# Optimization experiments

Hardware: AMD Instinct MI355X
Metric: run time of the kernel (lower is better)

## Reference

```python
import jax, jax.numpy as jnp
import numpy as np

NB, HD, NL, NF = 5, 64, 4, 10           # num_bins, hidden_dim(d_model), num_layers, num_frames
DI, DS, DC, DTR = 128, 16, 4, 4          # d_inner=2*HD, d_state, d_conv, dt_rank=ceil(HD/16)
B, H, W = 4, 64, 64


def _conv2d(x, w, b):
    y = jax.lax.conv_general_dilated(x, w, (1, 1), 'SAME',
                                     dimension_numbers=('NCHW', 'OIHW', 'NCHW'))
    return y + b[None, :, None, None]


def _bn_relu(x, gamma, beta, eps=1e-5):
    # BatchNorm2d in training mode: biased batch stats over (N,H,W)
    mean = x.mean(axis=(0, 2, 3), keepdims=True)
    var = x.var(axis=(0, 2, 3), keepdims=True)
    y = (x - mean) * jax.lax.rsqrt(var + eps)
    return jax.nn.relu(y * gamma[None, :, None, None] + beta[None, :, None, None])


def _silu(x):
    return x * jax.nn.sigmoid(x)


def _causal_dwconv(x, w, b):
    # x: (B,L,DI), w: (DI,K) depthwise causal conv, b: (DI,)
    K = w.shape[1]
    L = x.shape[1]
    xp = jnp.pad(x, ((0, 0), (K - 1, 0), (0, 0)))
    y = sum(xp[:, k:k + L, :] * w[:, k] for k in range(K))
    return y + b


def _selective_scan(u, delta, A, Bm, Cm, D):
    # u,delta: (B,L,DI); A: (DI,DS); Bm,Cm: (B,L,DS); D: (DI,)
    dT, BT, CT, uT = (t.transpose(1, 0, 2) for t in (delta, Bm, Cm, u))
    h0 = jnp.zeros((u.shape[0], A.shape[0], A.shape[1]), u.dtype)

    def step(h, inp):
        d_t, B_t, C_t, u_t = inp                     # (B,DI),(B,DS),(B,DS),(B,DI)
        dA = jnp.exp(d_t[:, :, None] * A)            # (B,DI,DS)
        h = dA * h + (d_t * u_t)[:, :, None] * B_t[:, None, :]
        y = jnp.einsum('bds,bs->bd', h, C_t)
        return h, y

    _, ys = jax.lax.scan(step, h0, (dT, BT, CT, uT))  # ys: (L,B,DI)
    return ys.transpose(1, 0, 2) + u * D


def _mamba(x, in_proj, conv_w, conv_b, x_proj, dt_w, dt_b, A_log, Dp, out_proj):
    xz = x @ in_proj.T                               # (B,L,2*DI)
    xi, z = jnp.split(xz, 2, axis=-1)
    xi = _silu(_causal_dwconv(xi, conv_w, conv_b))
    xdbc = xi @ x_proj.T                             # (B,L,DTR+2*DS)
    dt, Bm, Cm = jnp.split(xdbc, [DTR, DTR + DS], axis=-1)
    delta = jax.nn.softplus(dt @ dt_w.T + dt_b)
    A = -jnp.exp(A_log)
    y = _selective_scan(xi, delta, A, Bm, Cm, Dp)
    return (y * _silu(z)) @ out_proj.T


def setup_inputs() -> dict:
    key = jax.random.key(0)
    ks = jax.random.split(key, 20)
    s = 0.02
    inp = {
        'x': jax.random.normal(ks[0], (B, NB, H, W), jnp.float32),
        'enc_w': jax.random.normal(ks[1], (HD, NB, 3, 3), jnp.float32) * s,
        'enc_b': jnp.zeros((HD,), jnp.float32),
        'enc_g': jnp.ones((HD,), jnp.float32),
        'enc_be': jnp.zeros((HD,), jnp.float32),
        'in_proj': jax.random.normal(ks[2], (NL, 2 * DI, HD), jnp.float32) * s,
        'conv_w': jax.random.normal(ks[3], (NL, DI, DC), jnp.float32) * s,
        'conv_b': jnp.zeros((NL, DI), jnp.float32),
        'x_proj': jax.random.normal(ks[4], (NL, DTR + 2 * DS, DI), jnp.float32) * s,
        'dt_w': jax.random.normal(ks[5], (NL, DI, DTR), jnp.float32) * s,
        'dt_b': jax.random.normal(ks[6], (NL, DI), jnp.float32) * 0.1 - 4.0,
        'A_log': jnp.broadcast_to(jnp.log(jnp.arange(1, DS + 1, dtype=jnp.float32)),
                                  (NL, DI, DS)).copy(),
        'Dp': jnp.ones((NL, DI), jnp.float32),
        'out_proj': jax.random.normal(ks[7], (NL, HD, DI), jnp.float32) * s,
        'dec1_w': jax.random.normal(ks[8], (HD, HD, 3, 3), jnp.float32) * s,
        'dec1_b': jnp.zeros((HD,), jnp.float32),
        'dec1_g': jnp.ones((HD,), jnp.float32),
        'dec1_be': jnp.zeros((HD,), jnp.float32),
        'dec2_w': jax.random.normal(ks[9], (NF, HD, 3, 3), jnp.float32) * s,
        'dec2_b': jnp.zeros((NF,), jnp.float32),
    }
    return inp


def reference(x, enc_w, enc_b, enc_g, enc_be, in_proj, conv_w, conv_b, x_proj,
              dt_w, dt_b, A_log, Dp, out_proj, dec1_w, dec1_b, dec1_g, dec1_be,
              dec2_w, dec2_b):
    Bb, _, Hh, Ww = x.shape
    h = _bn_relu(_conv2d(x, enc_w, enc_b), enc_g, enc_be)   # (B,HD,H,W)
    t = h.reshape(Bb, HD, Hh * Ww).transpose(0, 2, 1)        # (B,L,HD)
    for i in range(NL):
        t = t + _mamba(t, in_proj[i], conv_w[i], conv_b[i], x_proj[i],
                       dt_w[i], dt_b[i], A_log[i], Dp[i], out_proj[i])
    h = t.transpose(0, 2, 1).reshape(Bb, HD, Hh, Ww)
    h = _bn_relu(_conv2d(h, dec1_w, dec1_b), dec1_g, dec1_be)
    return _conv2d(h, dec2_w, dec2_b)                        # (B,NF,H,W)
```

## Files before the change

kernel.cpp:

```cpp
#include <hip/hip_runtime.h>
#include <hip/hip_bf16.h>

#define BB   4
#define NBC  5
#define HD   64
#define NLAYER 4
#define NFC  10
#define DIM  128
#define DSN  16
#define DCN  4
#define DTRK 4
#define HH   64
#define WWD  64
#define LL   4096
#define MM   (BB*LL)
#define NCHUNK 128
#define CLEN   32
#define TSTEP  16

__global__ void k_prep_all(const float* __restrict__ in_proj, const float* __restrict__ out_proj,
                           const float* __restrict__ dec1_w, const float* __restrict__ dec2_w,
                           float* __restrict__ wTin, float* __restrict__ wTout,
                           float* __restrict__ wT1, float* __restrict__ wT2,
                           float* __restrict__ stats, float* __restrict__ stats2) {
    int idx = blockIdx.x * blockDim.x + threadIdx.x;
    if (idx < 65536) {
        int n = idx & 255, k = (idx >> 8) & 63, l = idx >> 14;
        wTin[idx] = in_proj[(l << 14) + (n << 6) + k];
    } else if (idx < 98304) {
        int j = idx - 65536;
        int n = j & 63, k = (j >> 6) & 127, l = j >> 13;
        wTout[j] = out_proj[(l << 13) + (n << 7) + k];
    } else if (idx < 135168) {
        int j = idx - 98304;
        int co = j & 63, tap = (j >> 6) % 9, ci = j / 576;
        wT1[j] = dec1_w[co * 576 + ci * 9 + tap];
    } else if (idx < 142848) {
        int j = idx - 135168;
        int tap = j % 12, t2 = j / 12, co = t2 % NFC, ci = t2 / NFC;
        wT2[j] = (tap < 9) ? dec2_w[co * 576 + ci * 9 + tap] : 0.f;
    } else if (idx < 143104) {
        int j = idx - 142848;
        if (j < 128) stats[j] = 0.f; else stats2[j - 128] = 0.f;
    }
}

__global__ void k_enc_conv(const float* __restrict__ x, const float* __restrict__ w,
                           const float* __restrict__ bias, float* __restrict__ out,
                           float* __restrict__ stats) {
    __shared__ float r1[256], r2[256];
    int tid = threadIdx.x;
    int idx = blockIdx.x * 256 + tid;
    int wx = idx & 63;
    int hy = (idx >> 6) & 63;
    int co = (idx >> 12) & 63;
    int b  = idx >> 18;
    float acc = bias[co];
    for (int ci = 0; ci < NBC; ++ci) {
        const float* xin = x + (((long)(b * NBC + ci)) << 12);
        const float* wp  = w + (co * NBC + ci) * 9;
        #pragma unroll
        for (int kh = 0; kh < 3; ++kh) {
            int ih = hy + kh - 1;
            if (ih < 0 || ih >= HH) continue;
            #pragma unroll
            for (int kw = 0; kw < 3; ++kw) {
                int iw = wx + kw - 1;
                if (iw < 0 || iw >= WWD) continue;
                acc += xin[(ih << 6) + iw] * wp[kh * 3 + kw];
            }
        }
    }
    out[idx] = acc;
    r1[tid] = acc; r2[tid] = acc * acc;
    __syncthreads();
    for (int off = 128; off > 0; off >>= 1) {
        if (tid < off) { r1[tid] += r1[tid + off]; r2[tid] += r2[tid + off]; }
        __syncthreads();
    }
    if (tid == 0) {
        atomicAdd(&stats[co], r1[0]);
        atomicAdd(&stats[64 + co], r2[0]);
    }
}

__global__ __launch_bounds__(256, 1) void k_gemm_in_bn(const float* __restrict__ src,
                                                       const float* __restrict__ stats,
                                                       const float* __restrict__ g,
                                                       const float* __restrict__ be,
                                                       const float* __restrict__ wT,
                                                       float* __restrict__ tout,
                                                       float* __restrict__ xz) {
    __shared__ __align__(16) float ts[64 * 68];
    __shared__ float sc[64], sh[64];
    long m0 = (long)blockIdx.x << 6;
    int b = (int)(m0 >> 12);
    int hw0 = (int)(m0 & 4095);
    int tid = threadIdx.x;
    if (tid < 64) {
        float m = stats[tid] * (1.f / 16384.f);
        float var = stats[64 + tid] * (1.f / 16384.f) - m * m;
        float ss = g[tid] * rsqrtf(var + 1e-5f);
        sc[tid] = ss; sh[tid] = be[tid] - m * ss;
    }
    __syncthreads();
    for (int i = tid; i < 4096; i += 256) {
        int pix = i & 63, c = i >> 6;
        float v = src[(((long)((b << 6) + c)) << 12) + hw0 + pix];
        ts[pix * 68 + c] = fmaxf(v * sc[c] + sh[c], 0.f);
    }
    __syncthreads();
    for (int i = tid; i < 4096; i += 256) {
        int r = i >> 6, c = i & 63;
        tout[(m0 + r) * 64 + c] = ts[r * 68 + c];
    }
    int rg = tid >> 5;
    int cg = tid & 31;
    float acc[8][8] = {};
    int n0 = cg << 3;
    for (int k4 = 0; k4 < 16; ++k4) {
        float4 a[8];
        #pragma unroll
        for (int r2 = 0; r2 < 8; ++r2)
            a[r2] = *(const float4*)&ts[((rg << 3) + r2) * 68 + (k4 << 2)];
        #pragma unroll
        for (int kk = 0; kk < 4; ++kk) {
            const float* wr = wT + (((k4 << 2) + kk) << 8) + n0;
            float4 w0 = *(const float4*)&wr[0];
            float4 w1 = *(const float4*)&wr[4];
            #pragma unroll
            for (int r2 = 0; r2 < 8; ++r2) {
                float av = (kk == 0) ? a[r2].x : (kk == 1) ? a[r2].y
                         : (kk == 2) ? a[r2].z : a[r2].w;
                acc[r2][0] += av * w0.x; acc[r2][1] += av * w0.y;
                acc[r2][2] += av * w0.z; acc[r2][3] += av * w0.w;
                acc[r2][4] += av * w1.x; acc[r2][5] += av * w1.y;
                acc[r2][6] += av * w1.z; acc[r2][7] += av * w1.w;
            }
        }
    }
    #pragma unroll
    for (int r2 = 0; r2 < 8; ++r2) {
        long m = m0 + (rg << 3) + r2;
        *(float4*)&xz[(m << 8) + n0]     = make_float4(acc[r2][0], acc[r2][1], acc[r2][2], acc[r2][3]);
        *(float4*)&xz[(m << 8) + n0 + 4] = make_float4(acc[r2][4], acc[r2][5], acc[r2][6], acc[r2][7]);
    }
}

__global__ __launch_bounds__(256, 2) void k_xproj_fused(
        const float* __restrict__ xz, const float* __restrict__ cw,
        const float* __restrict__ cb, const float* __restrict__ Wx,
        const float* __restrict__ dw, const float* __restrict__ dbias,
        const float* __restrict__ A_log,
        float* __restrict__ xi, float* __restrict__ xdbc,
        float* __restrict__ delta, float* __restrict__ Pb, float* __restrict__ Sb) {
    __shared__ float xz_s[35 * 132];
    __shared__ float xi_s[32 * 132];
    __shared__ float w_s[36 * 132];
    __shared__ float xs[32 * 40];
    __shared__ float cwT[4 * 128];
    __shared__ float cb_s[128];
    long m0 = (long)blockIdx.x << 5;
    int l0 = (int)(m0 & 4095);
    int b = (int)(m0 >> 12);
    int chunk = l0 >> 5;
    int tid = threadIdx.x;

    for (int i = tid; i < 35 * 128; i += 256) {
        int j = i >> 7, k = i & 127;
        int l = l0 - 3 + j;
        float v = 0.f;
        if (l >= 0) v = xz[(m0 - 3 + j) * 256 + k];
        xz_s[j * 132 + k] = v;
    }
    if (tid < 128) cb_s[tid] = cb[tid];
    for (int i = tid; i < 512; i += 256) {
        int kk = i >> 7, di = i & 127;
        cwT[(kk << 7) + di] = cw[(di << 2) + kk];
    }
    for (int i = tid; i < 4608; i += 256) {
        int n = i >> 7, k = i & 127;
        w_s[n * 132 + k] = Wx[i];
    }
    __syncthreads();

    for (int ii = 0; ii < 4; ++ii) {
        int i = tid + (ii << 8);
        int r = i >> 5;
        int d4 = (i & 31) << 2;
        float4 a = *(const float4*)&cb_s[d4];
        #pragma unroll
        for (int kk = 0; kk < 4; ++kk) {
            float4 xv = *(const float4*)&xz_s[(r + kk) * 132 + d4];
            float4 wv = *(const float4*)&cwT[(kk << 7) + d4];
            a.x += xv.x * wv.x; a.y += xv.y * wv.y;
            a.z += xv.z * wv.z; a.w += xv.w * wv.w;
        }
        a.x = a.x / (1.f + __expf(-a.x));
        a.y = a.y / (1.f + __expf(-a.y));
        a.z = a.z / (1.f + __expf(-a.z));
        a.w = a.w / (1.f + __expf(-a.w));
        *(float4*)&xi_s[r * 132 + d4] = a;
        *(float4*)&xi[(m0 + r) * 128 + d4] = a;
    }
    __syncthreads();

    int n = tid & 63;
    int rg = tid >> 6;
    if (n < 36) {
        float acc[8] = {0,0,0,0,0,0,0,0};
        for (int k4 = 0; k4 < 32; ++k4) {
            float4 w4 = *(const float4*)&w_s[n * 132 + (k4 << 2)];
            #pragma unroll
            for (int r = 0; r < 8; ++r) {
                float4 a4 = *(const float4*)&xi_s[((rg << 3) + r) * 132 + (k4 << 2)];
                acc[r] += a4.x * w4.x + a4.y * w4.y + a4.z * w4.z + a4.w * w4.w;
            }
        }
        #pragma unroll
        for (int r = 0; r < 8; ++r) {
            int rr = (rg << 3) + r;
            xdbc[(m0 + rr) * 36 + n] = acc[r];
            xs[rr * 40 + n] = acc[r];
        }
    }
    __syncthreads();

    float* delta_s = xz_s;
    for (int i = tid; i < 4096; i += 256) {
        int r = i >> 7, di = i & 127;
        float v = dbias[di];
        float4 d4 = *(const float4*)&dw[di << 2];
        v += xs[r * 40 + 0] * d4.x + xs[r * 40 + 1] * d4.y
           + xs[r * 40 + 2] * d4.z + xs[r * 40 + 3] * d4.w;
        float sp = (v > 20.f) ? v : log1pf(expf(v));
        delta[(m0 + r) * 128 + di] = sp;
        delta_s[r * 132 + di] = sp;
    }
    __syncthreads();

    {
        int di = tid >> 1;
        int dso = (tid & 1) << 3;
        float4 al0 = *(const float4*)&A_log[(di << 4) + dso];
        float4 al1 = *(const float4*)&A_log[(di << 4) + dso + 4];
        float Av[8] = { -expf(al0.x), -expf(al0.y), -expf(al0.z), -expf(al0.w),
                        -expf(al1.x), -expf(al1.y), -expf(al1.z), -expf(al1.w) };
        float h[8] = {0,0,0,0,0,0,0,0};
        float P[8] = {1,1,1,1,1,1,1,1};
        #pragma unroll 4
        for (int i = 0; i < CLEN; ++i) {
            float d = delta_s[i * 132 + di];
            float u = xi_s[i * 132 + di];
            float du = d * u;
            float4 B0 = *(float4*)&xs[i * 40 + DTRK + dso];
            float4 B1 = *(float4*)&xs[i * 40 + DTRK + dso + 4];
            float a0 = __expf(d * Av[0]); h[0] = a0 * h[0] + du * B0.x; P[0] *= a0;
            float a1 = __expf(d * Av[1]); h[1] = a1 * h[1] + du * B0.y; P[1] *= a1;
            float a2 = __expf(d * Av[2]); h[2] = a2 * h[2] + du * B0.z; P[2] *= a2;
            float a3 = __expf(d * Av[3]); h[3] = a3 * h[3] + du * B0.w; P[3] *= a3;
            float a4 = __expf(d * Av[4]); h[4] = a4 * h[4] + du * B1.x; P[4] *= a4;
            float a5 = __expf(d * Av[5]); h[5] = a5 * h[5] + du * B1.y; P[5] *= a5;
            float a6 = __expf(d * Av[6]); h[6] = a6 * h[6] + du * B1.z; P[6] *= a6;
            float a7 = __expf(d * Av[7]); h[7] = a7 * h[7] + du * B1.w; P[7] *= a7;
        }
        long o = (((long)chunk * BB + b) << 11) + (di << 4) + dso;
        *(float4*)&Pb[o]     = make_float4(P[0], P[1], P[2], P[3]);
        *(float4*)&Pb[o + 4] = make_float4(P[4], P[5], P[6], P[7]);
        *(float4*)&Sb[o]     = make_float4(h[0], h[1], h[2], h[3]);
        *(float4*)&Sb[o + 4] = make_float4(h[4], h[5], h[6], h[7]);
    }
}

__global__ void k_scan_p2(float* Pb, const float* __restrict__ Sb) {
    int t = blockIdx.x * blockDim.x + threadIdx.x;
    int b = t >> 11;
    int s = t & 2047;
    float h = 0.f;
    for (int c = 0; c < NCHUNK; ++c) {
        long idx = (((long)c * BB + b) << 11) + s;
        float p = Pb[idx];
        float sv = Sb[idx];
        Pb[idx] = h;
        h = p * h + sv;
    }
}

__global__ __launch_bounds__(256, 1) void k_scan_p3_oi(
        const float* __restrict__ delta, const float* __restrict__ xi,
        const float* __restrict__ xdbc, const float* __restrict__ A_log,
        const float* __restrict__ Dp, const float* __restrict__ xz,
        const float* __restrict__ hin, const float* __restrict__ wTo,
        const float* __restrict__ wTi, float* __restrict__ tio,
        float* __restrict__ xz_out, int doB) {
    __shared__ __align__(16) float d_s[32 * 132];
    __shared__ __align__(16) float u_s[32 * 132];
    __shared__ __align__(16) float bc_s[32 * 36];
    __shared__ __align__(16) float t_s[32 * 68];
    int chunk = blockIdx.x, b = blockIdx.y;
    int tid = threadIdx.x;
    long t0 = ((long)b << 12) + (long)chunk * CLEN;

    for (int i = tid; i < 1024; i += 256) {
        int r = i >> 5, c4 = (i & 31) << 2;
        *(float4*)&d_s[r * 132 + c4] = *(const float4*)&delta[(t0 + r) * 128 + c4];
        *(float4*)&u_s[r * 132 + c4] = *(const float4*)&xi[(t0 + r) * 128 + c4];
    }
    {
        int r = tid >> 3, c4 = (tid & 7) << 2;
        *(float4*)&bc_s[r * 36 + c4] = *(const float4*)&xdbc[(t0 + r) * 36 + DTRK + c4];
    }

    int di = tid >> 1;
    int dso = (tid & 1) << 3;
    float4 al0 = *(const float4*)&A_log[(di << 4) + dso];
    float4 al1 = *(const float4*)&A_log[(di << 4) + dso + 4];
    float Av[8] = { -expf(al0.x), -expf(al0.y), -expf(al0.z), -expf(al0.w),
                    -expf(al1.x), -expf(al1.y), -expf(al1.z), -expf(al1.w) };
    float Dv = Dp[di];
    long o = (((long)chunk * BB + b) << 11) + (di << 4) + dso;
    float4 h0 = *(const float4*)&hin[o];
    float4 h1 = *(const float4*)&hin[o + 4];
    float h[8] = { h0.x, h0.y, h0.z, h0.w, h1.x, h1.y, h1.z, h1.w };
    __syncthreads();

    #pragma unroll 4
    for (int i = 0; i < CLEN; ++i) {
        float d = d_s[i * 132 + di];
        float u = u_s[i * 132 + di];
        float du = d * u;
        const float* bc = &bc_s[i * 36];
        float4 B0 = *(const float4*)&bc[dso];
        float4 B1 = *(const float4*)&bc[dso + 4];
        float4 C0 = *(const float4*)&bc[16 + dso];
        float4 C1 = *(const float4*)&bc[16 + dso + 4];
        float a0 = __expf(d * Av[0]); h[0] = a0 * h[0] + du * B0.x;
        float a1 = __expf(d * Av[1]); h[1] = a1 * h[1] + du * B0.y;
        float a2 = __expf(d * Av[2]); h[2] = a2 * h[2] + du * B0.z;
        float a3 = __expf(d * Av[3]); h[3] = a3 * h[3] + du * B0.w;
        float a4 = __expf(d * Av[4]); h[4] = a4 * h[4] + du * B1.x;
        float a5 = __expf(d * Av[5]); h[5] = a5 * h[5] + du * B1.y;
        float a6 = __expf(d * Av[6]); h[6] = a6 * h[6] + du * B1.z;
        float a7 = __expf(d * Av[7]); h[7] = a7 * h[7] + du * B1.w;
        float yp = h[0] * C0.x + h[1] * C0.y + h[2] * C0.z + h[3] * C0.w
                 + h[4] * C1.x + h[5] * C1.y + h[6] * C1.z + h[7] * C1.w;
        yp += __shfl_xor(yp, 1);
        if (dso == 0)
            u_s[i * 132 + di] = yp + u * Dv;
    }
    __syncthreads();

    for (int i = tid; i < 1024; i += 256) {
        int r = i >> 5, c4 = (i & 31) << 2;
        float4 y4 = *(float4*)&u_s[r * 132 + c4];
        float4 z4 = *(const float4*)&xz[((t0 + r) << 8) + DIM + c4];
        y4.x *= z4.x / (1.f + __expf(-z4.x));
        y4.y *= z4.y / (1.f + __expf(-z4.y));
        y4.z *= z4.z / (1.f + __expf(-z4.z));
        y4.w *= z4.w / (1.f + __expf(-z4.w));
        *(float4*)&u_s[r * 132 + c4] = y4;
    }
    __syncthreads();

    {
        int rg = tid >> 4, cg = tid & 15;
        int n0 = cg << 2;
        float acc[2][4] = {};
        for (int k4 = 0; k4 < 32; ++k4) {
            float4 a0 = *(const float4*)&u_s[(rg << 1) * 132 + (k4 << 2)];
            float4 a1 = *(const float4*)&u_s[((rg << 1) + 1) * 132 + (k4 << 2)];
            #pragma unroll
            for (int kk = 0; kk < 4; ++kk) {
                const float* wr = wTo + (((k4 << 2) + kk) << 6) + n0;
                float4 w0 = *(const float4*)&wr[0];
                float av0 = (kk == 0) ? a0.x : (kk == 1) ? a0.y : (kk == 2) ? a0.z : a0.w;
                float av1 = (kk == 0) ? a1.x : (kk == 1) ? a1.y : (kk == 2) ? a1.z : a1.w;
                acc[0][0] += av0 * w0.x; acc[0][1] += av0 * w0.y;
                acc[0][2] += av0 * w0.z; acc[0][3] += av0 * w0.w;
                acc[1][0] += av1 * w0.x; acc[1][1] += av1 * w0.y;
                acc[1][2] += av1 * w0.z; acc[1][3] += av1 * w0.w;
            }
        }
        #pragma unroll
        for (int r2 = 0; r2 < 2; ++r2) {
            long m = t0 + (rg << 1) + r2;
            float4 tv = *(const float4*)&tio[(m << 6) + n0];
            tv.x += acc[r2][0]; tv.y += acc[r2][1];
            tv.z += acc[r2][2]; tv.w += acc[r2][3];
            *(float4*)&tio[(m << 6) + n0] = tv;
            *(float4*)&t_s[((rg << 1) + r2) * 68 + n0] = tv;
        }
    }
    if (!doB) return;
    __syncthreads();

    {
        int rg = tid >> 5, cgn = tid & 31;
        int n0 = cgn << 3;
        float acc[4][8] = {};
        for (int k4 = 0; k4 < 16; ++k4) {
            float4 a[4];
            #pragma unroll
            for (int r2 = 0; r2 < 4; ++r2)
                a[r2] = *(const float4*)&t_s[((rg << 2) + r2) * 68 + (k4 << 2)];
            #pragma unroll
            for (int kk = 0; kk < 4; ++kk) {
                const float* wr = wTi + (((k4 << 2) + kk) << 8) + n0;
                float4 w0 = *(const float4*)&wr[0];
                float4 w1 = *(const float4*)&wr[4];
                #pragma unroll
                for (int r2 = 0; r2 < 4; ++r2) {
                    float av = (kk == 0) ? a[r2].x : (kk == 1) ? a[r2].y
                             : (kk == 2) ? a[r2].z : a[r2].w;
                    acc[r2][0] += av * w0.x; acc[r2][1] += av * w0.y;
                    acc[r2][2] += av * w0.z; acc[r2][3] += av * w0.w;
                    acc[r2][4] += av * w1.x; acc[r2][5] += av * w1.y;
                    acc[r2][6] += av * w1.z; acc[r2][7] += av * w1.w;
                }
            }
        }
        #pragma unroll
        for (int r2 = 0; r2 < 4; ++r2) {
            long m = t0 + (rg << 2) + r2;
            *(float4*)&xz_out[(m << 8) + n0]     = make_float4(acc[r2][0], acc[r2][1], acc[r2][2], acc[r2][3]);
            *(float4*)&xz_out[(m << 8) + n0 + 4] = make_float4(acc[r2][4], acc[r2][5], acc[r2][6], acc[r2][7]);
        }
    }
}

__global__ __launch_bounds__(256, 1) void k_dec1_new(const float* __restrict__ tin,
                                                     const float* __restrict__ wT,
                                                     const float* __restrict__ bias,
                                                     float* __restrict__ out,
                                                     float* __restrict__ stats2) {
    __shared__ __align__(16) float x_s[64 * 132];
    __shared__ __align__(16) float w_s[4 * 4608];
    int tile = blockIdx.x;
    int b = blockIdx.y;
    int ty0 = (tile >> 3) << 3;
    int tx0 = (tile & 7) << 3;
    int tid = threadIdx.x;
    int wv = tid >> 6;
    int lane = tid & 63;
    int r = lane >> 3;
    int cg = lane & 7;

    for (int i = tid; i < 6400; i += 256) {
        int pl = i >> 6;
        int c = i & 63;
        int py = pl / 10, px = pl - py * 10;
        int ih = ty0 + py - 1, iw = tx0 + px - 1;
        float v = 0.f;
        if (ih >= 0 && ih < HH && iw >= 0 && iw < WWD)
            v = tin[(((long)((b << 12) + (ih << 6) + iw)) << 6) + c];
        x_s[c * 132 + py * 12 + px] = v;
    }
    float* myw = &w_s[wv * 4608];
    const float* gw = wT + (wv * 16) * 576;
    float4 pref[18];
    #pragma unroll
    for (int i = 0; i < 18; ++i)
        pref[i] = *(const float4*)&gw[(i * 64 + lane) * 4];
    #pragma unroll
    for (int i = 0; i < 18; ++i)
        *(float4*)&myw[(i * 64 + lane) * 4] = pref[i];
    __syncthreads();

    float acc[8][8] = {};
    #pragma unroll
    for (int ch = 0; ch < 2; ++ch) {
        if (ch == 0) {
            const float* gw1 = wT + (wv * 16 + 8) * 576;
            #pragma unroll
            for (int i = 0; i < 18; ++i)
                pref[i] = *(const float4*)&gw1[(i * 64 + lane) * 4];
        }
        for (int cl = 0; cl < 8; ++cl) {
            int cib = wv * 16 + ch * 8 + cl;
            float xrow[3][10];
            #pragma unroll
            for (int kh = 0; kh < 3; ++kh) {
                const float* xr = &x_s[cib * 132 + (r + kh) * 12];
                float4 a0 = *(const float4*)&xr[0];
                float4 a1 = *(const float4*)&xr[4];
                float2 a2 = *(const float2*)&xr[8];
                xrow[kh][0] = a0.x; xrow[kh][1] = a0.y; xrow[kh][2] = a0.z; xrow[kh][3] = a0.w;
                xrow[kh][4] = a1.x; xrow[kh][5] = a1.y; xrow[kh][6] = a1.z; xrow[kh][7] = a1.w;
                xrow[kh][8] = a2.x; xrow[kh][9] = a2.y;
            }
            const float* wp = &myw[cl * 576];
            #pragma unroll
            for (int kh = 0; kh < 3; ++kh) {
                #pragma unroll
                for (int kw = 0; kw < 3; ++kw) {
                    const float* wp2 = wp + (kh * 3 + kw) * 64 + (cg << 3);
                    float4 wa = *(const float4*)&wp2[0];
                    float4 wb = *(const float4*)&wp2[4];
                    #pragma unroll
                    for (int j = 0; j < 8; ++j) {
                        float xv = xrow[kh][kw + j];
                        acc[j][0] += xv * wa.x; acc[j][1] += xv * wa.y;
                        acc[j][2] += xv * wa.z; acc[j][3] += xv * wa.w;
                        acc[j][4] += xv * wb.x; acc[j][5] += xv * wb.y;
                        acc[j][6] += xv * wb.z; acc[j][7] += xv * wb.w;
                    }
                }
            }
        }
        if (ch == 0) {
            #pragma unroll
            for (int i = 0; i < 18; ++i)
                *(float4*)&myw[(i * 64 + lane) * 4] = pref[i];
        }
    }

    #pragma unroll
    for (int j = 0; j < 8; ++j) {
        *(float4*)&myw[lane * 68 + (j << 3)]     = make_float4(acc[j][0], acc[j][1], acc[j][2], acc[j][3]);
        *(float4*)&myw[lane * 68 + (j << 3) + 4] = make_float4(acc[j][4], acc[j][5], acc[j][6], acc[j][7]);
    }
    __syncthreads();

    float bv = bias[lane];
    float ssum = 0.f, ssq = 0.f;
    #pragma unroll
    for (int pp = 0; pp < 16; ++pp) {
        int pr = (wv << 1) + (pp >> 3);
        int pc = pp & 7;
        int ol = (pr << 3) + (lane >> 3);
        int ix = (pc << 3) + (lane & 7);
        float s = w_s[ol * 68 + ix] + w_s[4608 + ol * 68 + ix]
                + w_s[9216 + ol * 68 + ix] + w_s[13824 + ol * 68 + ix] + bv;
        out[(((long)((b << 12) + ((ty0 + pr) << 6) + tx0 + pc)) << 6) + lane] = s;
        ssum += s; ssq += s * s;
    }
    float* red = x_s;
    red[(wv << 6) + lane] = ssum;
    red[256 + (wv << 6) + lane] = ssq;
    __syncthreads();
    if (tid < 64) {
        float a = red[tid] + red[64 + tid] + red[128 + tid] + red[192 + tid];
        float q = red[256 + tid] + red[320 + tid] + red[384 + tid] + red[448 + tid];
        atomicAdd(&stats2[tid], a);
        atomicAdd(&stats2[64 + tid], q);
    }
}

__global__ void k_dec2_fused(const float* __restrict__ src, const float* __restrict__ stats2,
                             const float* __restrict__ g, const float* __restrict__ be,
                             const float* __restrict__ wT, const float* __restrict__ bias,
                             float* __restrict__ out) {
    __shared__ float x_s[64 * 101];
    __shared__ float w_s[64 * NFC * 12];
    __shared__ float sc_s[64];
    __shared__ float sh_s[64];
    int tile = blockIdx.x;
    int b = blockIdx.y;
    int ty0 = (tile >> 3) << 3;
    int tx0 = (tile & 7) << 3;
    int tid = threadIdx.x;

    if (tid < 64) {
        float m = stats2[tid] * (1.f / 16384.f);
        float var = stats2[64 + tid] * (1.f / 16384.f) - m * m;
        float s = g[tid] * rsqrtf(var + 1e-5f);
        sc_s[tid] = s;
        sh_s[tid] = be[tid] - m * s;
    }
    for (int i = tid; i < 64 * NFC * 12; i += 256)
        w_s[i] = wT[i];
    __syncthreads();

    for (int i = tid; i < 6400; i += 256) {
        int pl = i >> 6;
        int c = i & 63;
        int py = pl / 10, px = pl - py * 10;
        int ih = ty0 + py - 1, iw = tx0 + px - 1;
        float v = 0.f;
        if (ih >= 0 && ih < HH && iw >= 0 && iw < WWD) {
            v = src[((long)((b << 12) + (ih << 6) + iw)) * 64 + c];
            v = fmaxf(v * sc_s[c] + sh_s[c], 0.f);
        }
        x_s[c * 101 + pl] = v;
    }
    __syncthreads();

    int px = tid & 63;
    int py = px >> 3, pxx = px & 7;
    int cog = tid >> 6;
    float acc[3] = {0.f, 0.f, 0.f};
    int nco = (cog < 2) ? 3 : 2;

    for (int ci = 0; ci < 64; ++ci) {
        const float* xr = &x_s[ci * 101 + py * 10 + pxx];
        float xv[9];
        #pragma unroll
        for (int kh = 0; kh < 3; ++kh)
            #pragma unroll
            for (int kw = 0; kw < 3; ++kw)
                xv[kh * 3 + kw] = xr[kh * 10 + kw];
        #pragma unroll
        for (int j = 0; j < 3; ++j) {
            if (j >= nco) break;
            int co = cog + (j << 2);
            const float* wp = &w_s[(ci * NFC + co) * 12];
            float4 w0 = *(const float4*)&wp[0];
            float4 w1 = *(const float4*)&wp[4];
            float  w8 = wp[8];
            acc[j] += xv[0] * w0.x + xv[1] * w0.y + xv[2] * w0.z + xv[3] * w0.w
                    + xv[4] * w1.x + xv[5] * w1.y + xv[6] * w1.z + xv[7] * w1.w
                    + xv[8] * w8;
        }
    }
    int hw = ((ty0 + py) << 6) + tx0 + pxx;
    #pragma unroll
    for (int j = 0; j < 3; ++j) {
        if (j >= nco) break;
        int co = cog + (j << 2);
        out[((long)(b * NFC + co) << 12) + hw] = acc[j] + bias[co];
    }
}

extern "C" void kernel_launch(void* const* d_in, const int* in_sizes, int n_in,
                              void* d_out, int out_size, void* d_ws, size_t ws_size,
                              hipStream_t stream) {
    const float* x       = (const float*)d_in[0];
    const float* enc_w   = (const float*)d_in[1];
    const float* enc_b   = (const float*)d_in[2];
    const float* enc_g   = (const float*)d_in[3];
    const float* enc_be  = (const float*)d_in[4];
    const float* in_proj = (const float*)d_in[5];
    const float* conv_w  = (const float*)d_in[6];
    const float* conv_b  = (const float*)d_in[7];
    const float* x_proj  = (const float*)d_in[8];
    const float* dt_w    = (const float*)d_in[9];
    const float* dt_b    = (const float*)d_in[10];
    const float* A_log   = (const float*)d_in[11];
    const float* Dp      = (const float*)d_in[12];
    const float* out_prj = (const float*)d_in[13];
    const float* dec1_w  = (const float*)d_in[14];
    const float* dec1_b  = (const float*)d_in[15];
    const float* dec1_g  = (const float*)d_in[16];
    const float* dec1_be = (const float*)d_in[17];
    const float* dec2_w  = (const float*)d_in[18];
    const float* dec2_b  = (const float*)d_in[19];
    float* out = (float*)d_out;

    float* ws = (float*)d_ws;
    size_t off = 0;
    float* conv_buf  = ws + off; off += 1048576;
    float* stats     = ws + off; off += 128;
    float* stats2    = ws + off; off += 128;
    float* wT1       = ws + off; off += 36864;
    float* wT2       = ws + off; off += 7680;
    float* wTin      = ws + off; off += 65536;
    float* wTout     = ws + off; off += 32768;
    float* t_buf     = ws + off; off += 1048576;
    float* xz_buf    = ws + off; off += 4194304;
    float* xi_buf    = ws + off; off += 2097152;
    float* xdbc_buf  = ws + off; off += 589824;
    float* delta_buf = ws + off; off += 2097152;
    float* Sb_buf    = ws + off; off += 1048576;
    (void)ws_size; (void)in_sizes; (void)n_in; (void)out_size;

    float* Pb = conv_buf;
    float* Sb = Sb_buf;

    k_prep_all<<<560, 256, 0, stream>>>(in_proj, out_prj, dec1_w, dec2_w,
                                        wTin, wTout, wT1, wT2, stats, stats2);

    k_enc_conv<<<4096, 256, 0, stream>>>(x, enc_w, enc_b, conv_buf, stats);

    k_gemm_in_bn<<<256, 256, 0, stream>>>(conv_buf, stats, enc_g, enc_be, wTin, t_buf, xz_buf);
    dim3 pg(NCHUNK, BB);
    for (int i = 0; i < NLAYER; ++i) {
        k_xproj_fused<<<512, 256, 0, stream>>>(xz_buf, conv_w + i * DIM * DCN,
                                               conv_b + i * DIM, x_proj + i * 36 * DIM,
                                               dt_w + i * DIM * DTRK, dt_b + i * DIM,
                                               A_log + i * DIM * DSN,
                                               xi_buf, xdbc_buf, delta_buf, Pb, Sb);
        k_scan_p2<<<32, 256, 0, stream>>>(Pb, Sb);
        int doB = (i < NLAYER - 1) ? 1 : 0;
        k_scan_p3_oi<<<pg, 256, 0, stream>>>(delta_buf, xi_buf, xdbc_buf,
                                             A_log + i * DIM * DSN, Dp + i * DIM,
                                             xz_buf, Pb, wTout + i * 8192,
                                             wTin + ((i + 1) & 3) * 16384,
                                             t_buf, xz_buf, doB);
    }

    dim3 dg1(64, BB);
    k_dec1_new<<<dg1, 256, 0, stream>>>(t_buf, wT1, dec1_b, conv_buf, stats2);
    k_dec2_fused<<<dg1, 256, 0, stream>>>(conv_buf, stats2, dec1_g, dec1_be, wT2, dec2_b, out);
}
```

Baseline: 490.9 us.

## Recompute conv/delta in scan pass and shrink chunks with halo buffers

Stops writing xi and delta to global memory and recomputes the causal depthwise conv, SiLU and softplus delta inside the scan output kernel. Because xz is overwritten in place by the next layer's in-projection, the last three rows of each 16-step subchunk are saved to ping-pong halo buffers for the conv window. Chunk length drops from 32 to 16, giving twice as many blocks, with occupancy hints raised. The aim is to cut global memory traffic and improve parallelism, at the cost of duplicated arithmetic and a sequential inter-chunk pass that is now twice as long.

```diff
diff --git a/kernel.cpp b/kernel.cpp
--- a/kernel.cpp
+++ b/kernel.cpp
@@ -14,9 +14,9 @@
 #define WWD  64
 #define LL   4096
 #define MM   (BB*LL)
-#define NCHUNK 128
-#define CLEN   32
-#define TSTEP  16
+#define SUB    16
+#define NSUB   256
+#define WIN    19
 
 __global__ void k_prep_all(const float* __restrict__ in_proj, const float* __restrict__ out_proj,
                            const float* __restrict__ dec1_w, const float* __restrict__ dec2_w,
@@ -90,7 +90,8 @@
                                                        const float* __restrict__ be,
                                                        const float* __restrict__ wT,
                                                        float* __restrict__ tout,
-                                                       float* __restrict__ xz) {
+                                                       float* __restrict__ xz,
+                                                       float* __restrict__ halo0) {
     __shared__ __align__(16) float ts[64 * 68];
     __shared__ float sc[64], sh[64];
     long m0 = (long)blockIdx.x << 6;
@@ -142,100 +143,106 @@
     #pragma unroll
     for (int r2 = 0; r2 < 8; ++r2) {
         long m = m0 + (rg << 3) + r2;
-        *(float4*)&xz[(m << 8) + n0]     = make_float4(acc[r2][0], acc[r2][1], acc[r2][2], acc[r2][3]);
-        *(float4*)&xz[(m << 8) + n0 + 4] = make_float4(acc[r2][4], acc[r2][5], acc[r2][6], acc[r2][7]);
-    }
-}
-
-__global__ __launch_bounds__(256, 2) void k_xproj_fused(
+        float4 v0 = make_float4(acc[r2][0], acc[r2][1], acc[r2][2], acc[r2][3]);
+        float4 v1 = make_float4(acc[r2][4], acc[r2][5], acc[r2][6], acc[r2][7]);
+        *(float4*)&xz[(m << 8) + n0]     = v0;
+        *(float4*)&xz[(m << 8) + n0 + 4] = v1;
+        int lr = (int)(m & 15);
+        if (lr >= 13 && n0 < 128) {
+            int bb = (int)(m >> 12), scc = ((int)m & 4095) >> 4;
+            long ho = (((long)bb * NSUB + scc) * 3 + (lr - 13)) * 128 + n0;
+            *(float4*)&halo0[ho]     = v0;
+            *(float4*)&halo0[ho + 4] = v1;
+        }
+    }
+}
+
+__global__ __launch_bounds__(256, 3) void k_xproj_fused(
         const float* __restrict__ xz, const float* __restrict__ cw,
         const float* __restrict__ cb, const float* __restrict__ Wx,
         const float* __restrict__ dw, const float* __restrict__ dbias,
         const float* __restrict__ A_log,
-        float* __restrict__ xi, float* __restrict__ xdbc,
-        float* __restrict__ delta, float* __restrict__ Pb, float* __restrict__ Sb) {
-    __shared__ float xz_s[35 * 132];
-    __shared__ float xi_s[32 * 132];
-    __shared__ float w_s[36 * 132];
-    __shared__ float xs[32 * 40];
-    __shared__ float cwT[4 * 128];
-    __shared__ float cb_s[128];
-    long m0 = (long)blockIdx.x << 5;
+        float* __restrict__ xdbc, float* __restrict__ Pb, float* __restrict__ Sb) {
+    __shared__ __align__(16) float xz_s[WIN * 128];
+    __shared__ __align__(16) float xi_s[SUB * 128];
+    __shared__ __align__(16) float w_s[36 * 132];
+    __shared__ __align__(16) float xs[SUB * 36];
+    long m0 = (long)blockIdx.x << 4;
     int l0 = (int)(m0 & 4095);
     int b = (int)(m0 >> 12);
-    int chunk = l0 >> 5;
+    int sc = l0 >> 4;
     int tid = threadIdx.x;
 
-    for (int i = tid; i < 35 * 128; i += 256) {
-        int j = i >> 7, k = i & 127;
+    for (int i = tid; i < WIN * 32; i += 256) {
+        int j = i >> 5, c4 = (i & 31) << 2;
+        float4 v = make_float4(0.f, 0.f, 0.f, 0.f);
         int l = l0 - 3 + j;
-        float v = 0.f;
-        if (l >= 0) v = xz[(m0 - 3 + j) * 256 + k];
-        xz_s[j * 132 + k] = v;
-    }
-    if (tid < 128) cb_s[tid] = cb[tid];
-    for (int i = tid; i < 512; i += 256) {
-        int kk = i >> 7, di = i & 127;
-        cwT[(kk << 7) + di] = cw[(di << 2) + kk];
-    }
-    for (int i = tid; i < 4608; i += 256) {
-        int n = i >> 7, k = i & 127;
-        w_s[n * 132 + k] = Wx[i];
-    }
-    __syncthreads();
-
-    for (int ii = 0; ii < 4; ++ii) {
-        int i = tid + (ii << 8);
-        int r = i >> 5;
-        int d4 = (i & 31) << 2;
-        float4 a = *(const float4*)&cb_s[d4];
-        #pragma unroll
-        for (int kk = 0; kk < 4; ++kk) {
-            float4 xv = *(const float4*)&xz_s[(r + kk) * 132 + d4];
-            float4 wv = *(const float4*)&cwT[(kk << 7) + d4];
-            a.x += xv.x * wv.x; a.y += xv.y * wv.y;
-            a.z += xv.z * wv.z; a.w += xv.w * wv.w;
-        }
+        if (l >= 0) v = *(const float4*)&xz[(m0 - 3 + j) * 256 + c4];
+        *(float4*)&xz_s[j * 128 + c4] = v;
+    }
+    for (int i = tid; i < 1152; i += 256) {
+        int n = i >> 5, c4 = (i & 31) << 2;
+        *(float4*)&w_s[n * 132 + c4] = *(const float4*)&Wx[(n << 7) + c4];
+    }
+    int d4c = (tid & 31) << 2;
+    float4 cwv0 = *(const float4*)&cw[(d4c + 0) << 2];
+    float4 cwv1 = *(const float4*)&cw[(d4c + 1) << 2];
+    float4 cwv2 = *(const float4*)&cw[(d4c + 2) << 2];
+    float4 cwv3 = *(const float4*)&cw[(d4c + 3) << 2];
+    float4 cbv  = *(const float4*)&cb[d4c];
+    __syncthreads();
+
+    #pragma unroll
+    for (int ii = 0; ii < 2; ++ii) {
+        int r = (tid >> 5) + (ii << 3);
+        float4 x0 = *(const float4*)&xz_s[(r + 0) * 128 + d4c];
+        float4 x1 = *(const float4*)&xz_s[(r + 1) * 128 + d4c];
+        float4 x2 = *(const float4*)&xz_s[(r + 2) * 128 + d4c];
+        float4 x3 = *(const float4*)&xz_s[(r + 3) * 128 + d4c];
+        float4 a;
+        a.x = cbv.x + x0.x * cwv0.x + x1.x * cwv0.y + x2.x * cwv0.z + x3.x * cwv0.w;
+        a.y = cbv.y + x0.y * cwv1.x + x1.y * cwv1.y + x2.y * cwv1.z + x3.y * cwv1.w;
+        a.z = cbv.z + x0.z * cwv2.x + x1.z * cwv2.y + x2.z * cwv2.z + x3.z * cwv2.w;
+        a.w = cbv.w + x0.w * cwv3.x + x1.w * cwv3.y + x2.w * cwv3.z + x3.w * cwv3.w;
         a.x = a.x / (1.f + __expf(-a.x));
         a.y = a.y / (1.f + __expf(-a.y));
         a.z = a.z / (1.f + __expf(-a.z));
         a.w = a.w / (1.f + __expf(-a.w));
-        *(float4*)&xi_s[r * 132 + d4] = a;
-        *(float4*)&xi[(m0 + r) * 128 + d4] = a;
-    }
-    __syncthreads();
-
-    int n = tid & 63;
-    int rg = tid >> 6;
-    if (n < 36) {
-        float acc[8] = {0,0,0,0,0,0,0,0};
-        for (int k4 = 0; k4 < 32; ++k4) {
-            float4 w4 = *(const float4*)&w_s[n * 132 + (k4 << 2)];
-            #pragma unroll
-            for (int r = 0; r < 8; ++r) {
-                float4 a4 = *(const float4*)&xi_s[((rg << 3) + r) * 132 + (k4 << 2)];
-                acc[r] += a4.x * w4.x + a4.y * w4.y + a4.z * w4.z + a4.w * w4.w;
-            }
-        }
-        #pragma unroll
-        for (int r = 0; r < 8; ++r) {
-            int rr = (rg << 3) + r;
-            xdbc[(m0 + rr) * 36 + n] = acc[r];
-            xs[rr * 40 + n] = acc[r];
+        *(float4*)&xi_s[r * 128 + d4c] = a;
+    }
+    __syncthreads();
+
+    {
+        int n = tid & 63, rg6 = tid >> 6;
+        if (n < 36) {
+            float acc[4] = {0, 0, 0, 0};
+            for (int k4 = 0; k4 < 32; ++k4) {
+                float4 w4 = *(const float4*)&w_s[n * 132 + (k4 << 2)];
+                #pragma unroll
+                for (int r = 0; r < 4; ++r) {
+                    float4 a4 = *(const float4*)&xi_s[((rg6 << 2) + r) * 128 + (k4 << 2)];
+                    acc[r] += a4.x * w4.x + a4.y * w4.y + a4.z * w4.z + a4.w * w4.w;
+                }
+            }
+            #pragma unroll
+            for (int r = 0; r < 4; ++r) {
+                int rr = (rg6 << 2) + r;
+                xdbc[(m0 + rr) * 36 + n] = acc[r];
+                xs[rr * 36 + n] = acc[r];
+            }
         }
     }
     __syncthreads();
 
     float* delta_s = xz_s;
-    for (int i = tid; i < 4096; i += 256) {
-        int r = i >> 7, di = i & 127;
-        float v = dbias[di];
-        float4 d4 = *(const float4*)&dw[di << 2];
-        v += xs[r * 40 + 0] * d4.x + xs[r * 40 + 1] * d4.y
-           + xs[r * 40 + 2] * d4.z + xs[r * 40 + 3] * d4.w;
+    for (int i = tid; i < SUB * 128; i += 256) {
+        int r = i >> 7, di2 = i & 127;
+        float4 d4 = *(const float4*)&dw[di2 << 2];
+        float v = dbias[di2]
+                + xs[r * 36 + 0] * d4.x + xs[r * 36 + 1] * d4.y
+                + xs[r * 36 + 2] * d4.z + xs[r * 36 + 3] * d4.w;
         float sp = (v > 20.f) ? v : log1pf(expf(v));
-        delta[(m0 + r) * 128 + di] = sp;
-        delta_s[r * 132 + di] = sp;
+        delta_s[r * 128 + di2] = sp;
     }
     __syncthreads();
 
@@ -249,12 +256,12 @@
         float h[8] = {0,0,0,0,0,0,0,0};
         float P[8] = {1,1,1,1,1,1,1,1};
         #pragma unroll 4
-        for (int i = 0; i < CLEN; ++i) {
-            float d = delta_s[i * 132 + di];
-            float u = xi_s[i * 132 + di];
+        for (int i = 0; i < SUB; ++i) {
+            float d = delta_s[i * 128 + di];
+            float u = xi_s[i * 128 + di];
             float du = d * u;
-            float4 B0 = *(float4*)&xs[i * 40 + DTRK + dso];
-            float4 B1 = *(float4*)&xs[i * 40 + DTRK + dso + 4];
+            float4 B0 = *(const float4*)&xs[i * 36 + DTRK + dso];
+            float4 B1 = *(const float4*)&xs[i * 36 + DTRK + dso + 4];
             float a0 = __expf(d * Av[0]); h[0] = a0 * h[0] + du * B0.x; P[0] *= a0;
             float a1 = __expf(d * Av[1]); h[1] = a1 * h[1] + du * B0.y; P[1] *= a1;
             float a2 = __expf(d * Av[2]); h[2] = a2 * h[2] + du * B0.z; P[2] *= a2;
@@ -264,7 +271,7 @@
             float a6 = __expf(d * Av[6]); h[6] = a6 * h[6] + du * B1.z; P[6] *= a6;
             float a7 = __expf(d * Av[7]); h[7] = a7 * h[7] + du * B1.w; P[7] *= a7;
         }
-        long o = (((long)chunk * BB + b) << 11) + (di << 4) + dso;
+        long o = (((long)(b * NSUB + sc)) << 11) + (di << 4) + dso;
         *(float4*)&Pb[o]     = make_float4(P[0], P[1], P[2], P[3]);
         *(float4*)&Pb[o + 4] = make_float4(P[4], P[5], P[6], P[7]);
         *(float4*)&Sb[o]     = make_float4(h[0], h[1], h[2], h[3]);
@@ -272,45 +279,61 @@
     }
 }
 
-__global__ void k_scan_p2(float* Pb, const float* __restrict__ Sb) {
+__global__ void k_scan_p2(const float* __restrict__ Pb, float* Sb) {
     int t = blockIdx.x * blockDim.x + threadIdx.x;
     int b = t >> 11;
     int s = t & 2047;
     float h = 0.f;
-    for (int c = 0; c < NCHUNK; ++c) {
-        long idx = (((long)c * BB + b) << 11) + s;
-        float p = Pb[idx];
-        float sv = Sb[idx];
-        Pb[idx] = h;
-        h = p * h + sv;
-    }
-}
-
-__global__ __launch_bounds__(256, 1) void k_scan_p3_oi(
-        const float* __restrict__ delta, const float* __restrict__ xi,
-        const float* __restrict__ xdbc, const float* __restrict__ A_log,
-        const float* __restrict__ Dp, const float* __restrict__ xz,
-        const float* __restrict__ hin, const float* __restrict__ wTo,
-        const float* __restrict__ wTi, float* __restrict__ tio,
-        float* __restrict__ xz_out, int doB) {
-    __shared__ __align__(16) float d_s[32 * 132];
-    __shared__ __align__(16) float u_s[32 * 132];
-    __shared__ __align__(16) float bc_s[32 * 36];
-    __shared__ __align__(16) float t_s[32 * 68];
-    int chunk = blockIdx.x, b = blockIdx.y;
+    for (int c = 0; c < 128; ++c) {
+        long i0 = (((long)((b << 8) + (c << 1))) << 11) + s;
+        long i1 = i0 + 2048;
+        float p0 = Pb[i0], s0 = Sb[i0];
+        float p1 = Pb[i1], s1 = Sb[i1];
+        Sb[i0] = h;
+        float h1 = p0 * h + s0;
+        Sb[i1] = h1;
+        h = p1 * h1 + s1;
+    }
+}
+
+__global__ __launch_bounds__(256, 4) void k_scan_p3_oi(
+        float* xz, const float* __restrict__ xdbc,
+        const float* __restrict__ cw, const float* __restrict__ cb,
+        const float* __restrict__ dw, const float* __restrict__ dbias,
+        const float* __restrict__ A_log, const float* __restrict__ Dp,
+        const float* __restrict__ wTo, const float* __restrict__ wTi,
+        float* __restrict__ tio, const float* __restrict__ h0g,
+        const float* __restrict__ haloIn, float* __restrict__ haloOut, int doB) {
+    __shared__ __align__(16) float xw_s[WIN * 128];
+    __shared__ __align__(16) float u_s[SUB * 132];
+    __shared__ __align__(16) float bc_s[SUB * 36];
+    __shared__ __align__(16) float t_s[SUB * 68];
+    long m0 = (long)blockIdx.x << 4;
+    int l0 = (int)(m0 & 4095);
+    int b = (int)(m0 >> 12);
+    int sc = l0 >> 4;
     int tid = threadIdx.x;
-    long t0 = ((long)b << 12) + (long)chunk * CLEN;
-
-    for (int i = tid; i < 1024; i += 256) {
-        int r = i >> 5, c4 = (i & 31) << 2;
-        *(float4*)&d_s[r * 132 + c4] = *(const float4*)&delta[(t0 + r) * 128 + c4];
-        *(float4*)&u_s[r * 132 + c4] = *(const float4*)&xi[(t0 + r) * 128 + c4];
-    }
-    {
-        int r = tid >> 3, c4 = (tid & 7) << 2;
-        *(float4*)&bc_s[r * 36 + c4] = *(const float4*)&xdbc[(t0 + r) * 36 + DTRK + c4];
-    }
-
+    int fb = b * NSUB + sc;
+
+    for (int i = tid; i < WIN * 32; i += 256) {
+        int j = i >> 5, c4 = (i & 31) << 2;
+        float4 v = make_float4(0.f, 0.f, 0.f, 0.f);
+        if (j >= 3)
+            v = *(const float4*)&xz[(m0 + j - 3) * 256 + c4];
+        else if (sc > 0)
+            v = *(const float4*)&haloIn[(((long)fb - 1) * 3 + j) * 128 + c4];
+        *(float4*)&xw_s[j * 128 + c4] = v;
+    }
+    for (int i = tid; i < SUB * 9; i += 256) {
+        int r = i / 9, c4 = (i - r * 9) << 2;
+        *(float4*)&bc_s[r * 36 + c4] = *(const float4*)&xdbc[(m0 + r) * 36 + c4];
+    }
+    int d4c = (tid & 31) << 2;
+    float4 cwv0 = *(const float4*)&cw[(d4c + 0) << 2];
+    float4 cwv1 = *(const float4*)&cw[(d4c + 1) << 2];
+    float4 cwv2 = *(const float4*)&cw[(d4c + 2) << 2];
+    float4 cwv3 = *(const float4*)&cw[(d4c + 3) << 2];
+    float4 cbv  = *(const float4*)&cb[d4c];
     int di = tid >> 1;
     int dso = (tid & 1) << 3;
     float4 al0 = *(const float4*)&A_log[(di << 4) + dso];
@@ -318,22 +341,54 @@
     float Av[8] = { -expf(al0.x), -expf(al0.y), -expf(al0.z), -expf(al0.w),
                     -expf(al1.x), -expf(al1.y), -expf(al1.z), -expf(al1.w) };
     float Dv = Dp[di];
-    long o = (((long)chunk * BB + b) << 11) + (di << 4) + dso;
-    float4 h0 = *(const float4*)&hin[o];
-    float4 h1 = *(const float4*)&hin[o + 4];
-    float h[8] = { h0.x, h0.y, h0.z, h0.w, h1.x, h1.y, h1.z, h1.w };
+    long o = (((long)fb) << 11) + (di << 4) + dso;
+    float4 h04 = *(const float4*)&h0g[o];
+    float4 h14 = *(const float4*)&h0g[o + 4];
+    float h[8] = { h04.x, h04.y, h04.z, h04.w, h14.x, h14.y, h14.z, h14.w };
+    __syncthreads();
+
+    #pragma unroll
+    for (int ii = 0; ii < 2; ++ii) {
+        int r = (tid >> 5) + (ii << 3);
+        float4 x0 = *(const float4*)&xw_s[(r + 0) * 128 + d4c];
+        float4 x1 = *(const float4*)&xw_s[(r + 1) * 128 + d4c];
+        float4 x2 = *(const float4*)&xw_s[(r + 2) * 128 + d4c];
+        float4 x3 = *(const float4*)&xw_s[(r + 3) * 128 + d4c];
+        float4 a;
+        a.x = cbv.x + x0.x * cwv0.x + x1.x * cwv0.y + x2.x * cwv0.z + x3.x * cwv0.w;
+        a.y = cbv.y + x0.y * cwv1.x + x1.y * cwv1.y + x2.y * cwv1.z + x3.y * cwv1.w;
+        a.z = cbv.z + x0.z * cwv2.x + x1.z * cwv2.y + x2.z * cwv2.z + x3.z * cwv2.w;
+        a.w = cbv.w + x0.w * cwv3.x + x1.w * cwv3.y + x2.w * cwv3.z + x3.w * cwv3.w;
+        a.x = a.x / (1.f + __expf(-a.x));
+        a.y = a.y / (1.f + __expf(-a.y));
+        a.z = a.z / (1.f + __expf(-a.z));
+        a.w = a.w / (1.f + __expf(-a.w));
+        *(float4*)&u_s[r * 132 + d4c] = a;
+    }
+    __syncthreads();
+
+    float* delta_s = xw_s;
+    for (int i = tid; i < SUB * 128; i += 256) {
+        int r = i >> 7, di2 = i & 127;
+        float4 d4 = *(const float4*)&dw[di2 << 2];
+        float v = dbias[di2]
+                + bc_s[r * 36 + 0] * d4.x + bc_s[r * 36 + 1] * d4.y
+                + bc_s[r * 36 + 2] * d4.z + bc_s[r * 36 + 3] * d4.w;
+        float sp = (v > 20.f) ? v : log1pf(expf(v));
+        delta_s[r * 128 + di2] = sp;
+    }
     __syncthreads();
 
     #pragma unroll 4
-    for (int i = 0; i < CLEN; ++i) {
-        float d = d_s[i * 132 + di];
+    for (int i = 0; i < SUB; ++i) {
+        float d = delta_s[i * 128 + di];
         float u = u_s[i * 132 + di];
         float du = d * u;
         const float* bc = &bc_s[i * 36];
-        float4 B0 = *(const float4*)&bc[dso];
-        float4 B1 = *(const float4*)&bc[dso + 4];
-        float4 C0 = *(const float4*)&bc[16 + dso];
-        float4 C1 = *(const float4*)&bc[16 + dso + 4];
+        float4 B0 = *(const float4*)&bc[DTRK + dso];
+        float4 B1 = *(const float4*)&bc[DTRK + dso + 4];
+        float4 C0 = *(const float4*)&bc[DTRK + DSN + dso];
+        float4 C1 = *(const float4*)&bc[DTRK + DSN + dso + 4];
         float a0 = __expf(d * Av[0]); h[0] = a0 * h[0] + du * B0.x;
         float a1 = __expf(d * Av[1]); h[1] = a1 * h[1] + du * B0.y;
         float a2 = __expf(d * Av[2]); h[2] = a2 * h[2] + du * B0.z;
@@ -350,10 +405,10 @@
     }
     __syncthreads();
 
-    for (int i = tid; i < 1024; i += 256) {
+    for (int i = tid; i < SUB * 32; i += 256) {
         int r = i >> 5, c4 = (i & 31) << 2;
         float4 y4 = *(float4*)&u_s[r * 132 + c4];
-        float4 z4 = *(const float4*)&xz[((t0 + r) << 8) + DIM + c4];
+        float4 z4 = *(const float4*)&xz[((m0 + r) << 8) + DIM + c4];
         y4.x *= z4.x / (1.f + __expf(-z4.x));
         y4.y *= z4.y / (1.f + __expf(-z4.y));
         y4.z *= z4.z / (1.f + __expf(-z4.z));
@@ -362,7 +417,7 @@
     }
     __syncthreads();
 
-    {
+    if (tid < 128) {
         int rg = tid >> 4, cg = tid & 15;
         int n0 = cg << 2;
         float acc[2][4] = {};
@@ -383,7 +438,7 @@
         }
         #pragma unroll
         for (int r2 = 0; r2 < 2; ++r2) {
-            long m = t0 + (rg << 1) + r2;
+            long m = m0 + (rg << 1) + r2;
             float4 tv = *(const float4*)&tio[(m << 6) + n0];
             tv.x += acc[r2][0]; tv.y += acc[r2][1];
             tv.z += acc[r2][2]; tv.w += acc[r2][3];
@@ -397,19 +452,18 @@
     {
         int rg = tid >> 5, cgn = tid & 31;
         int n0 = cgn << 3;
-        float acc[4][8] = {};
+        float acc[2][8] = {};
         for (int k4 = 0; k4 < 16; ++k4) {
-            float4 a[4];
-            #pragma unroll
-            for (int r2 = 0; r2 < 4; ++r2)
-                a[r2] = *(const float4*)&t_s[((rg << 2) + r2) * 68 + (k4 << 2)];
+            float4 a[2];
+            a[0] = *(const float4*)&t_s[(rg << 1) * 68 + (k4 << 2)];
+            a[1] = *(const float4*)&t_s[((rg << 1) + 1) * 68 + (k4 << 2)];
             #pragma unroll
             for (int kk = 0; kk < 4; ++kk) {
                 const float* wr = wTi + (((k4 << 2) + kk) << 8) + n0;
                 float4 w0 = *(const float4*)&wr[0];
                 float4 w1 = *(const float4*)&wr[4];
                 #pragma unroll
-                for (int r2 = 0; r2 < 4; ++r2) {
+                for (int r2 = 0; r2 < 2; ++r2) {
                     float av = (kk == 0) ? a[r2].x : (kk == 1) ? a[r2].y
                              : (kk == 2) ? a[r2].z : a[r2].w;
                     acc[r2][0] += av * w0.x; acc[r2][1] += av * w0.y;
@@ -420,10 +474,18 @@
             }
         }
         #pragma unroll
-        for (int r2 = 0; r2 < 4; ++r2) {
-            long m = t0 + (rg << 2) + r2;
-            *(float4*)&xz_out[(m << 8) + n0]     = make_float4(acc[r2][0], acc[r2][1], acc[r2][2], acc[r2][3]);
-            *(float4*)&xz_out[(m << 8) + n0 + 4] = make_float4(acc[r2][4], acc[r2][5], acc[r2][6], acc[r2][7]);
+        for (int r2 = 0; r2 < 2; ++r2) {
+            long m = m0 + (rg << 1) + r2;
+            float4 v0 = make_float4(acc[r2][0], acc[r2][1], acc[r2][2], acc[r2][3]);
+            float4 v1 = make_float4(acc[r2][4], acc[r2][5], acc[r2][6], acc[r2][7]);
+            *(float4*)&xz[(m << 8) + n0]     = v0;
+            *(float4*)&xz[(m << 8) + n0 + 4] = v1;
+            int lr = (int)(m & 15);
+            if (lr >= 13 && n0 < 128) {
+                long ho = (((long)fb) * 3 + (lr - 13)) * 128 + n0;
+                *(float4*)&haloOut[ho]     = v0;
+                *(float4*)&haloOut[ho + 4] = v1;
+            }
         }
     }
 }
@@ -657,35 +719,35 @@
     float* wTout     = ws + off; off += 32768;
     float* t_buf     = ws + off; off += 1048576;
     float* xz_buf    = ws + off; off += 4194304;
-    float* xi_buf    = ws + off; off += 2097152;
     float* xdbc_buf  = ws + off; off += 589824;
-    float* delta_buf = ws + off; off += 2097152;
-    float* Sb_buf    = ws + off; off += 1048576;
+    float* Pb        = ws + off; off += 2097152;
+    float* Sb        = ws + off; off += 2097152;
+    float* halo0     = ws + off; off += 393216;
+    float* halo1     = ws + off; off += 393216;
     (void)ws_size; (void)in_sizes; (void)n_in; (void)out_size;
-
-    float* Pb = conv_buf;
-    float* Sb = Sb_buf;
 
     k_prep_all<<<560, 256, 0, stream>>>(in_proj, out_prj, dec1_w, dec2_w,
                                         wTin, wTout, wT1, wT2, stats, stats2);
 
     k_enc_conv<<<4096, 256, 0, stream>>>(x, enc_w, enc_b, conv_buf, stats);
 
-    k_gemm_in_bn<<<256, 256, 0, stream>>>(conv_buf, stats, enc_g, enc_be, wTin, t_buf, xz_buf);
-    dim3 pg(NCHUNK, BB);
+    k_gemm_in_bn<<<256, 256, 0, stream>>>(conv_buf, stats, enc_g, enc_be, wTin,
+                                          t_buf, xz_buf, halo0);
+
     for (int i = 0; i < NLAYER; ++i) {
-        k_xproj_fused<<<512, 256, 0, stream>>>(xz_buf, conv_w + i * DIM * DCN,
-                                               conv_b + i * DIM, x_proj + i * 36 * DIM,
-                                               dt_w + i * DIM * DTRK, dt_b + i * DIM,
-                                               A_log + i * DIM * DSN,
-                                               xi_buf, xdbc_buf, delta_buf, Pb, Sb);
+        const float* hin  = (i & 1) ? halo1 : halo0;
+        float* hout       = (i & 1) ? halo0 : halo1;
+        int doB = (i < NLAYER - 1) ? 1 : 0;
+        k_xproj_fused<<<1024, 256, 0, stream>>>(
+            xz_buf, conv_w + i * DIM * DCN, conv_b + i * DIM, x_proj + i * 36 * DIM,
+            dt_w + i * DIM * DTRK, dt_b + i * DIM, A_log + i * DIM * DSN,
+            xdbc_buf, Pb, Sb);
         k_scan_p2<<<32, 256, 0, stream>>>(Pb, Sb);
-        int doB = (i < NLAYER - 1) ? 1 : 0;
-        k_scan_p3_oi<<<pg, 256, 0, stream>>>(delta_buf, xi_buf, xdbc_buf,
-                                             A_log + i * DIM * DSN, Dp + i * DIM,
-                                             xz_buf, Pb, wTout + i * 8192,
-                                             wTin + ((i + 1) & 3) * 16384,
-                                             t_buf, xz_buf, doB);
+        k_scan_p3_oi<<<1024, 256, 0, stream>>>(
+            xz_buf, xdbc_buf, conv_w + i * DIM * DCN, conv_b + i * DIM,
+            dt_w + i * DIM * DTRK, dt_b + i * DIM, A_log + i * DIM * DSN, Dp + i * DIM,
+            wTout + i * 8192, wTin + ((i + 1) & 3) * 16384,
+            t_buf, Sb, hin, hout, doB);
     }
 
     dim3 dg1(64, BB);
```

Measured after the change: 1.233 ms. +151.1%, slower.
